# Kernel optimization log

Hardware: AMD Instinct MI355X
Metric: run time of the kernel (lower is better)

## Reference

```python
import jax, jax.numpy as jnp
import numpy as np

# Model dims (match init_kwargs)
H = 1024            # hidden_size
I = 2048            # intermediate_size (per expert)
NH = 16             # num_heads
HD = H // NH        # head_dim = 64
E = 8               # num_experts
TOPK = 2
MAX_SEQ = 2048
EPS = 1e-6
NEG = -1e9


def precompute_freqs_cis(dim, max_seq_len, theta=10000.0):
    # Faithful to source: cat([cos, sin], dim=-1) -> shape [S, dim]
    pos = np.arange(max_seq_len, dtype=np.float32)
    freqs = np.arange(0, dim, 2, dtype=np.float32) / dim
    inv_freq = 1.0 / (theta ** freqs)
    f = np.einsum('i,j->ij', pos, inv_freq)
    return jnp.asarray(np.concatenate([np.cos(f), np.sin(f)], axis=-1), dtype=jnp.float32)


def setup_inputs() -> dict:
    key = jax.random.key(0)
    ks = jax.random.split(key, 12)
    B, S = 2, 1024
    s = lambda fan: 1.0 / np.sqrt(fan)
    inp = {
        'x': jax.random.normal(ks[0], (B, S, H), dtype=jnp.float32),
        'attn_norm_w': jnp.ones((H,), dtype=jnp.float32),
        'ffn_norm_w': jnp.ones((H,), dtype=jnp.float32),
        'wq': jax.random.normal(ks[1], (H, H), dtype=jnp.float32) * s(H),
        'wk': jax.random.normal(ks[2], (H, H), dtype=jnp.float32) * s(H),
        'wv': jax.random.normal(ks[3], (H, H), dtype=jnp.float32) * s(H),
        'wo': jax.random.normal(ks[4], (H, H), dtype=jnp.float32) * s(H),
        'router_w': jax.random.normal(ks[5], (H, E), dtype=jnp.float32) * s(H),
        'w1': jax.random.normal(ks[6], (E, H, I), dtype=jnp.float32) * s(H),
        'w3': jax.random.normal(ks[7], (E, H, I), dtype=jnp.float32) * s(H),
        'w2': jax.random.normal(ks[8], (E, I, H), dtype=jnp.float32) * s(I),
        'freqs_cis': precompute_freqs_cis(HD, MAX_SEQ),
    }
    return inp


def rmsnorm(x, w):
    rms = jnp.sqrt(jnp.mean(x * x, axis=-1, keepdims=True) + EPS)
    return w * (x / rms)


def apply_rope(x, freqs_cis):
    # x: [B, S, NH, HD]; faithful to source pairing (interleaved view of cat(cos,sin))
    B, S, nh, hd = x.shape
    xr = x.reshape(B, S, nh, hd // 2, 2)
    fr = freqs_cis[:S].reshape(1, S, 1, hd // 2, 2)  # position_ids = arange(S)
    a, b = xr[..., 0], xr[..., 1]
    cr, ci = fr[..., 0], fr[..., 1]
    out = jnp.stack([a * cr - b * ci, a * ci + b * cr], axis=-1)
    return out.reshape(B, S, nh, hd)


def attention(x, wq, wk, wv, wo, freqs_cis):
    B, S, _ = x.shape
    q = (x @ wq).reshape(B, S, NH, HD)
    k = (x @ wk).reshape(B, S, NH, HD)
    v = (x @ wv).reshape(B, S, NH, HD)
    q = apply_rope(q, freqs_cis)
    k = apply_rope(k, freqs_cis)
    # [B, NH, S, S]
    scores = jnp.einsum('bqhd,bkhd->bhqk', q, k) / np.sqrt(HD).astype(np.float32)
    causal = jnp.tril(jnp.ones((S, S), dtype=bool))
    scores = jnp.where(causal[None, None], scores, NEG)
    attn = jax.nn.softmax(scores, axis=-1)
    out = jnp.einsum('bhqk,bkhd->bqhd', attn, v).reshape(B, S, H)
    return out @ wo


def moe_ffn(x, router_w, w1, w2, w3):
    # x: [B, S, H] -> flatten tokens
    B, S, _ = x.shape
    xt = x.reshape(B * S, H)                      # [T, H]
    logits = xt @ router_w                        # [T, E]
    probs = jax.nn.softmax(logits, axis=-1)
    topv, topi = jax.lax.top_k(probs, TOPK)       # [T, K]
    topv = topv / jnp.sum(topv, axis=-1, keepdims=True)  # renormalize top-k weights
    # combine[t, e] = sum_k topv[t,k] * 1[topi[t,k]==e]
    combine = jnp.sum(topv[..., None] * jax.nn.one_hot(topi, E, dtype=xt.dtype), axis=1)  # [T, E]
    # SwiGLU experts, dense over experts (mathematically identical to no-drop routing)
    h1 = jnp.einsum('th,ehi->eti', xt, w1)
    h3 = jnp.einsum('th,ehi->eti', xt, w3)
    ye = jnp.einsum('eti,eih->eth', jax.nn.silu(h1) * h3, w2)  # [E, T, H]
    out = jnp.einsum('te,eth->th', combine, ye)
    return out.reshape(B, S, H)


def reference(x, attn_norm_w, ffn_norm_w, wq, wk, wv, wo, router_w, w1, w3, w2, freqs_cis):
    h = x + attention(rmsnorm(x, attn_norm_w), wq, wk, wv, wo, freqs_cis)
    out = h + moe_ffn(rmsnorm(h, ffn_norm_w), router_w, w1, w2, w3)
    return out
```

## Files before the change

kernel.cpp:

```cpp
#include <hip/hip_runtime.h>
#include <hip/hip_bf16.h>
#include <math.h>

#define HS 1024
#define IS 2048
#define NHEAD 16
#define HDIM 64
#define NEXP 8
#define BATCH 2
#define SEQ 1024
#define NTOK (BATCH*SEQ)
#define NASSIGN (NTOK*2)
#define QKVW 3072
#define PAD 72

typedef short bf16x8 __attribute__((ext_vector_type(8)));
typedef float f32x4  __attribute__((ext_vector_type(4)));

__global__ void rmsnorm_split(const float* __restrict__ x, const float* __restrict__ w,
                              __hip_bfloat16* __restrict__ oh, __hip_bfloat16* __restrict__ ol) {
    int t = blockIdx.x;
    int tid = threadIdx.x;
    const float* row = x + (size_t)t * HS;
    float ss = 0.f;
    for (int i = tid; i < HS; i += 256) { float v = row[i]; ss += v * v; }
    for (int off = 32; off > 0; off >>= 1) ss += __shfl_down(ss, off);
    __shared__ float red[4];
    if ((tid & 63) == 0) red[tid >> 6] = ss;
    __syncthreads();
    float tot = red[0] + red[1] + red[2] + red[3];
    float rr = rsqrtf(tot / (float)HS + 1e-6f);
    for (int i = tid; i < HS; i += 256) {
        float v = w[i] * row[i] * rr;
        __hip_bfloat16 hi = __float2bfloat16(v);
        oh[(size_t)t * HS + i] = hi;
        ol[(size_t)t * HS + i] = __float2bfloat16(v - __bfloat162float(hi));
    }
}

__global__ void rmsnorm_dual(const float* __restrict__ x, const float* __restrict__ w,
                             float* __restrict__ outf, __hip_bfloat16* __restrict__ outb) {
    int t = blockIdx.x;
    int tid = threadIdx.x;
    const float* row = x + (size_t)t * HS;
    float ss = 0.f;
    for (int i = tid; i < HS; i += 256) { float v = row[i]; ss += v * v; }
    for (int off = 32; off > 0; off >>= 1) ss += __shfl_down(ss, off);
    __shared__ float red[4];
    if ((tid & 63) == 0) red[tid >> 6] = ss;
    __syncthreads();
    float tot = red[0] + red[1] + red[2] + red[3];
    float rr = rsqrtf(tot / (float)HS + 1e-6f);
    for (int i = tid; i < HS; i += 256) {
        float v = w[i] * row[i] * rr;
        outf[(size_t)t * HS + i] = v;
        outb[(size_t)t * HS + i] = __float2bfloat16(v);
    }
}

__global__ void transpose_split(const float* __restrict__ src,
                                __hip_bfloat16* __restrict__ dh, __hip_bfloat16* __restrict__ dl,
                                int R, int C, int rowOff) {
    __shared__ float tile[32][33];
    int c0 = blockIdx.x * 32, r0 = blockIdx.y * 32;
    int tx = threadIdx.x & 31, ty = threadIdx.x >> 5;
    #pragma unroll
    for (int i = 0; i < 4; i++) {
        int r = ty + i * 8;
        tile[r][tx] = src[(size_t)(r0 + r) * C + c0 + tx];
    }
    __syncthreads();
    #pragma unroll
    for (int i = 0; i < 4; i++) {
        int c = ty + i * 8;
        float v = tile[tx][c];
        __hip_bfloat16 hi = __float2bfloat16(v);
        size_t o = (size_t)(rowOff + c0 + c) * R + r0 + tx;
        dh[o] = hi;
        dl[o] = __float2bfloat16(v - __bfloat162float(hi));
    }
}

__global__ void transpose_bf16(const float* __restrict__ in, __hip_bfloat16* __restrict__ outp,
                               int R, int C) {
    __shared__ float tile[32][33];
    int e = blockIdx.z;
    const float* src = in + (size_t)e * R * C;
    __hip_bfloat16* dst = outp + (size_t)e * R * C;
    int c0 = blockIdx.x * 32, r0 = blockIdx.y * 32;
    int tx = threadIdx.x & 31, ty = threadIdx.x >> 5;
    #pragma unroll
    for (int i = 0; i < 4; i++) {
        int r = ty + i * 8;
        tile[r][tx] = src[(size_t)(r0 + r) * C + c0 + tx];
    }
    __syncthreads();
    #pragma unroll
    for (int i = 0; i < 4; i++) {
        int c = ty + i * 8;
        dst[(size_t)(c0 + c) * R + r0 + tx] = __float2bfloat16(tile[tx][c]);
    }
}

__global__ __launch_bounds__(256) void gemm_bf16x3(const __hip_bfloat16* __restrict__ Ah,
                                                   const __hip_bfloat16* __restrict__ Al,
                                                   const __hip_bfloat16* __restrict__ Bh,
                                                   const __hip_bfloat16* __restrict__ Bl,
                                                   const float* __restrict__ resid,
                                                   float* __restrict__ C,
                                                   int M, int N, int K) {
    __shared__ __align__(16) short Ahs[128][40];
    __shared__ __align__(16) short Als[128][40];
    __shared__ __align__(16) short Bhs[128][40];
    __shared__ __align__(16) short Bls[128][40];
    int bm = blockIdx.y * 128, bn = blockIdx.x * 128;
    int t = threadIdx.x;
    int wave = t >> 6, lane = t & 63;
    int wm = (wave & 1) * 64, wn = (wave >> 1) * 64;
    int fr = lane & 15;
    int kh = (lane >> 4) * 8;
    int srow = t >> 2;
    int scol = (t & 3) * 8;
    const __hip_bfloat16* a0h = Ah + (size_t)(bm + srow) * K + scol;
    const __hip_bfloat16* a1h = Ah + (size_t)(bm + 64 + srow) * K + scol;
    const __hip_bfloat16* a0l = Al + (size_t)(bm + srow) * K + scol;
    const __hip_bfloat16* a1l = Al + (size_t)(bm + 64 + srow) * K + scol;
    const __hip_bfloat16* b0h = Bh + (size_t)(bn + srow) * K + scol;
    const __hip_bfloat16* b1h = Bh + (size_t)(bn + 64 + srow) * K + scol;
    const __hip_bfloat16* b0l = Bl + (size_t)(bn + srow) * K + scol;
    const __hip_bfloat16* b1l = Bl + (size_t)(bn + 64 + srow) * K + scol;

    f32x4 acc[4][4] = {};
    for (int k0 = 0; k0 < K; k0 += 32) {
        *(uint4*)&Ahs[srow][scol]      = *(const uint4*)(a0h + k0);
        *(uint4*)&Ahs[64 + srow][scol] = *(const uint4*)(a1h + k0);
        *(uint4*)&Als[srow][scol]      = *(const uint4*)(a0l + k0);
        *(uint4*)&Als[64 + srow][scol] = *(const uint4*)(a1l + k0);
        *(uint4*)&Bhs[srow][scol]      = *(const uint4*)(b0h + k0);
        *(uint4*)&Bhs[64 + srow][scol] = *(const uint4*)(b1h + k0);
        *(uint4*)&Bls[srow][scol]      = *(const uint4*)(b0l + k0);
        *(uint4*)&Bls[64 + srow][scol] = *(const uint4*)(b1l + k0);
        __syncthreads();
        bf16x8 ah[4], bh[4], x[4];
        #pragma unroll
        for (int i = 0; i < 4; i++) {
            ah[i] = *(const bf16x8*)&Ahs[wm + i * 16 + fr][kh];
            bh[i] = *(const bf16x8*)&Bhs[wn + i * 16 + fr][kh];
        }
        #pragma unroll
        for (int mi = 0; mi < 4; mi++)
            #pragma unroll
            for (int ni = 0; ni < 4; ni++)
                acc[mi][ni] = __builtin_amdgcn_mfma_f32_16x16x32_bf16(ah[mi], bh[ni], acc[mi][ni], 0, 0, 0);
        #pragma unroll
        for (int i = 0; i < 4; i++) x[i] = *(const bf16x8*)&Bls[wn + i * 16 + fr][kh];
        #pragma unroll
        for (int mi = 0; mi < 4; mi++)
            #pragma unroll
            for (int ni = 0; ni < 4; ni++)
                acc[mi][ni] = __builtin_amdgcn_mfma_f32_16x16x32_bf16(ah[mi], x[ni], acc[mi][ni], 0, 0, 0);
        #pragma unroll
        for (int i = 0; i < 4; i++) x[i] = *(const bf16x8*)&Als[wm + i * 16 + fr][kh];
        #pragma unroll
        for (int mi = 0; mi < 4; mi++)
            #pragma unroll
            for (int ni = 0; ni < 4; ni++)
                acc[mi][ni] = __builtin_amdgcn_mfma_f32_16x16x32_bf16(x[mi], bh[ni], acc[mi][ni], 0, 0, 0);
        __syncthreads();
    }
    int rq = (lane >> 4) * 4;
    #pragma unroll
    for (int mi = 0; mi < 4; mi++) {
        #pragma unroll
        for (int r = 0; r < 4; r++) {
            size_t rowo = (size_t)(bm + wm + mi * 16 + rq + r) * N + bn + wn;
            #pragma unroll
            for (int ni = 0; ni < 4; ni++) {
                float v = acc[mi][ni][r];
                size_t o = rowo + ni * 16 + fr;
                if (resid) v += resid[o];
                C[o] = v;
            }
        }
    }
}

__global__ void rope_convert(const float* __restrict__ qkv, const float* __restrict__ fc,
                             __hip_bfloat16* __restrict__ qh, __hip_bfloat16* __restrict__ ql,
                             __hip_bfloat16* __restrict__ kh, __hip_bfloat16* __restrict__ kl,
                             __hip_bfloat16* __restrict__ vh, __hip_bfloat16* __restrict__ vl) {
    int t = blockIdx.x;
    int s = t & (SEQ - 1);
    const float* row = qkv + (size_t)t * QKVW;
    size_t ob = (size_t)t * HS;
    for (int p = threadIdx.x; p < 512; p += 256) {
        int hh = p >> 5, j = p & 31;
        int col = hh * 64 + 2 * j;
        float cr = fc[s * HDIM + 2 * j];
        float ci = fc[s * HDIM + 2 * j + 1];
        float a = row[col], b = row[col + 1];
        float r0 = a * cr - b * ci, r1 = a * ci + b * cr;
        __hip_bfloat16 h0 = __float2bfloat16(r0), h1 = __float2bfloat16(r1);
        qh[ob + col] = h0;     ql[ob + col]     = __float2bfloat16(r0 - __bfloat162float(h0));
        qh[ob + col + 1] = h1; ql[ob + col + 1] = __float2bfloat16(r1 - __bfloat162float(h1));
        a = row[1024 + col]; b = row[1024 + col + 1];
        r0 = a * cr - b * ci; r1 = a * ci + b * cr;
        h0 = __float2bfloat16(r0); h1 = __float2bfloat16(r1);
        kh[ob + col] = h0;     kl[ob + col]     = __float2bfloat16(r0 - __bfloat162float(h0));
        kh[ob + col + 1] = h1; kl[ob + col + 1] = __float2bfloat16(r1 - __bfloat162float(h1));
        r0 = row[2048 + col]; r1 = row[2048 + col + 1];
        h0 = __float2bfloat16(r0); h1 = __float2bfloat16(r1);
        vh[ob + col] = h0;     vl[ob + col]     = __float2bfloat16(r0 - __bfloat162float(h0));
        vh[ob + col + 1] = h1; vl[ob + col + 1] = __float2bfloat16(r1 - __bfloat162float(h1));
    }
}

__global__ __launch_bounds__(256) void attn_partial(
        const __hip_bfloat16* __restrict__ qh, const __hip_bfloat16* __restrict__ ql,
        const __hip_bfloat16* __restrict__ kh, const __hip_bfloat16* __restrict__ kl,
        const __hip_bfloat16* __restrict__ vh, const __hip_bfloat16* __restrict__ vl,
        float* __restrict__ po, float* __restrict__ pm_g, float* __restrict__ pl_g) {
    int c = blockIdx.x, qt = blockIdx.y;
    int nc = (qt + 4) >> 2;
    if (c >= nc) return;
    int bh = blockIdx.z;
    int b = bh >> 4, h = bh & 15;
    int t0 = c * 4, t1 = min(t0 + 4, qt + 1);
    int tid = threadIdx.x;
    int wave = tid >> 6, lane = tid & 63;
    int fr = lane & 15, quad = lane >> 4;
    int w16 = wave * 16;
    __shared__ __align__(16) short Qh[64][PAD], Ql[64][PAD];
    __shared__ __align__(16) short KPh[64][PAD], KPl[64][PAD];
    __shared__ __align__(16) short Vhs[64][PAD], Vls[64][PAD];
    size_t hoff = (size_t)h * HDIM;
    int sr = tid >> 2, sg = tid & 3;
    {
        const __hip_bfloat16* qp  = qh + (size_t)(b * SEQ + qt * 64 + sr) * HS + hoff;
        const __hip_bfloat16* qp2 = ql + (size_t)(b * SEQ + qt * 64 + sr) * HS + hoff;
        *(uint4*)&Qh[sr][sg * 8]       = *(const uint4*)(qp + sg * 8);
        *(uint4*)&Qh[sr][(sg + 4) * 8] = *(const uint4*)(qp + (sg + 4) * 8);
        *(uint4*)&Ql[sr][sg * 8]       = *(const uint4*)(qp2 + sg * 8);
        *(uint4*)&Ql[sr][(sg + 4) * 8] = *(const uint4*)(qp2 + (sg + 4) * 8);
    }
    f32x4 o[4] = {};
    float mrow[4], lrow[4];
    #pragma unroll
    for (int i = 0; i < 4; i++) { mrow[i] = -1e30f; lrow[i] = 0.f; }
    int key0 = (tid & 31) * 2, ds = tid >> 5;
    __syncthreads();

    for (int kt = t0; kt < t1; kt++) {
        int kbase = kt * 64;
        {
            const __hip_bfloat16* kp  = kh + (size_t)(b * SEQ + kbase + sr) * HS + hoff;
            const __hip_bfloat16* kp2 = kl + (size_t)(b * SEQ + kbase + sr) * HS + hoff;
            *(uint4*)&KPh[sr][sg * 8]       = *(const uint4*)(kp + sg * 8);
            *(uint4*)&KPh[sr][(sg + 4) * 8] = *(const uint4*)(kp + (sg + 4) * 8);
            *(uint4*)&KPl[sr][sg * 8]       = *(const uint4*)(kp2 + sg * 8);
            *(uint4*)&KPl[sr][(sg + 4) * 8] = *(const uint4*)(kp2 + (sg + 4) * 8);
        }
        {
            const __hip_bfloat16* v0 = vh + (size_t)(b * SEQ + kbase + key0) * HS + hoff + ds * 8;
            uint4 A = *(const uint4*)v0;
            uint4 Bv = *(const uint4*)(v0 + HS);
            const unsigned short* ap = (const unsigned short*)&A;
            const unsigned short* bp = (const unsigned short*)&Bv;
            #pragma unroll
            for (int j = 0; j < 8; j++)
                *(unsigned*)&Vhs[ds * 8 + j][key0] = (unsigned)ap[j] | ((unsigned)bp[j] << 16);
            const __hip_bfloat16* v2 = vl + (size_t)(b * SEQ + kbase + key0) * HS + hoff + ds * 8;
            uint4 A2 = *(const uint4*)v2;
            uint4 B2 = *(const uint4*)(v2 + HS);
            const unsigned short* ap2 = (const unsigned short*)&A2;
            const unsigned short* bp2 = (const unsigned short*)&B2;
            #pragma unroll
            for (int j = 0; j < 8; j++)
                *(unsigned*)&Vls[ds * 8 + j][key0] = (unsigned)ap2[j] | ((unsigned)bp2[j] << 16);
        }
        __syncthreads();

        f32x4 s[4] = {};
        #pragma unroll
        for (int ks = 0; ks < 2; ks++) {
            bf16x8 a_h = *(const bf16x8*)&Qh[w16 + fr][quad * 8 + ks * 32];
            bf16x8 a_l = *(const bf16x8*)&Ql[w16 + fr][quad * 8 + ks * 32];
            #pragma unroll
            for (int ni = 0; ni < 4; ni++) {
                bf16x8 b_h = *(const bf16x8*)&KPh[ni * 16 + fr][quad * 8 + ks * 32];
                bf16x8 b_l = *(const bf16x8*)&KPl[ni * 16 + fr][quad * 8 + ks * 32];
                s[ni] = __builtin_amdgcn_mfma_f32_16x16x32_bf16(a_h, b_h, s[ni], 0, 0, 0);
                s[ni] = __builtin_amdgcn_mfma_f32_16x16x32_bf16(a_h, b_l, s[ni], 0, 0, 0);
                s[ni] = __builtin_amdgcn_mfma_f32_16x16x32_bf16(a_l, b_h, s[ni], 0, 0, 0);
            }
        }
        int qg = qt * 64 + w16 + quad * 4;
        #pragma unroll
        for (int ni = 0; ni < 4; ni++) {
            int kg = kbase + ni * 16 + fr;
            #pragma unroll
            for (int r = 0; r < 4; r++)
                s[ni][r] = (kg > qg + r) ? -1e9f : s[ni][r] * 0.125f;
        }
        #pragma unroll
        for (int r = 0; r < 4; r++) {
            float mx = fmaxf(fmaxf(s[0][r], s[1][r]), fmaxf(s[2][r], s[3][r]));
            #pragma unroll
            for (int wd = 1; wd < 16; wd <<= 1) mx = fmaxf(mx, __shfl_xor(mx, wd));
            float nm = fmaxf(mrow[r], mx);
            float alpha = __expf(mrow[r] - nm);
            float rs = 0.f;
            #pragma unroll
            for (int ni = 0; ni < 4; ni++) { float e = __expf(s[ni][r] - nm); s[ni][r] = e; rs += e; }
            #pragma unroll
            for (int wd = 1; wd < 16; wd <<= 1) rs += __shfl_xor(rs, wd);
            lrow[r] = lrow[r] * alpha + rs;
            mrow[r] = nm;
            o[0][r] *= alpha; o[1][r] *= alpha; o[2][r] *= alpha; o[3][r] *= alpha;
        }
        __syncthreads();
        #pragma unroll
        for (int ni = 0; ni < 4; ni++)
            #pragma unroll
            for (int r = 0; r < 4; r++) {
                float pv = s[ni][r];
                __hip_bfloat16 hi = __float2bfloat16(pv);
                __hip_bfloat16 lo = __float2bfloat16(pv - __bfloat162float(hi));
                KPh[w16 + quad * 4 + r][ni * 16 + fr] = *(short*)&hi;
                KPl[w16 + quad * 4 + r][ni * 16 + fr] = *(short*)&lo;
            }
        #pragma unroll
        for (int ks = 0; ks < 2; ks++) {
            bf16x8 p_h = *(const bf16x8*)&KPh[w16 + fr][quad * 8 + ks * 32];
            bf16x8 p_l = *(const bf16x8*)&KPl[w16 + fr][quad * 8 + ks * 32];
            #pragma unroll
            for (int ni = 0; ni < 4; ni++) {
                bf16x8 v_h = *(const bf16x8*)&Vhs[ni * 16 + fr][quad * 8 + ks * 32];
                bf16x8 v_l = *(const bf16x8*)&Vls[ni * 16 + fr][quad * 8 + ks * 32];
                o[ni] = __builtin_amdgcn_mfma_f32_16x16x32_bf16(p_h, v_h, o[ni], 0, 0, 0);
                o[ni] = __builtin_amdgcn_mfma_f32_16x16x32_bf16(p_h, v_l, o[ni], 0, 0, 0);
                o[ni] = __builtin_amdgcn_mfma_f32_16x16x32_bf16(p_l, v_h, o[ni], 0, 0, 0);
            }
        }
        __syncthreads();
    }
    int pidx = (bh * 16 + qt) * 4 + c;
    float* pob = po + (size_t)pidx * 4096;
    #pragma unroll
    for (int ni = 0; ni < 4; ni++)
        #pragma unroll
        for (int r = 0; r < 4; r++)
            pob[(w16 + quad * 4 + r) * 64 + ni * 16 + fr] = o[ni][r];
    if (fr == 0) {
        #pragma unroll
        for (int r = 0; r < 4; r++) {
            pm_g[pidx * 64 + w16 + quad * 4 + r] = mrow[r];
            pl_g[pidx * 64 + w16 + quad * 4 + r] = lrow[r];
        }
    }
}

__global__ void attn_merge(const float* __restrict__ po, const float* __restrict__ pm,
                           const float* __restrict__ pl,
                           __hip_bfloat16* __restrict__ ch, __hip_bfloat16* __restrict__ cl) {
    int qt = blockIdx.x, h = blockIdx.y, b = blockIdx.z;
    int bh = b * 16 + h;
    int nc = (qt + 4) >> 2;
    int base = (bh * 16 + qt) * 4;
    int tid = threadIdx.x;
    int r  = tid >> 2;
    int d0 = (tid & 3) * 16;
    float mstar = -1e30f;
    for (int c = 0; c < nc; c++) mstar = fmaxf(mstar, pm[(base + c) * 64 + r]);
    float a[4];
    float lsum = 0.f;
    for (int c = 0; c < nc; c++) {
        a[c] = __expf(pm[(base + c) * 64 + r] - mstar);
        lsum += a[c] * pl[(base + c) * 64 + r];
    }
    float inv = 1.f / lsum;
    size_t crow = (size_t)(b * SEQ + qt * 64 + r) * HS + h * HDIM;
    for (int dd = 0; dd < 16; dd += 4) {
        float4 acc = make_float4(0.f, 0.f, 0.f, 0.f);
        for (int c = 0; c < nc; c++) {
            float4 v = *(const float4*)(po + (size_t)(base + c) * 4096 + r * 64 + d0 + dd);
            acc.x += a[c] * v.x; acc.y += a[c] * v.y;
            acc.z += a[c] * v.z; acc.w += a[c] * v.w;
        }
        float vs[4] = {acc.x * inv, acc.y * inv, acc.z * inv, acc.w * inv};
        #pragma unroll
        for (int j = 0; j < 4; j++) {
            __hip_bfloat16 hi = __float2bfloat16(vs[j]);
            ch[crow + d0 + dd + j] = hi;
            cl[crow + d0 + dd + j] = __float2bfloat16(vs[j] - __bfloat162float(hi));
        }
    }
}

__global__ void router_kernel(const float* __restrict__ hn, const float* __restrict__ rw,
                              int* __restrict__ cnt, int* __restrict__ topEk,
                              float* __restrict__ topW) {
    int t = blockIdx.x;
    int lane = threadIdx.x;
    float acc[NEXP];
    #pragma unroll
    for (int e = 0; e < NEXP; e++) acc[e] = 0.f;
    const float* row = hn + (size_t)t * HS;
    for (int kk = lane; kk < HS; kk += 64) {
        float xv = row[kk];
        const float* r = rw + (size_t)kk * NEXP;
        #pragma unroll
        for (int e = 0; e < NEXP; e++) acc[e] += xv * r[e];
    }
    #pragma unroll
    for (int e = 0; e < NEXP; e++)
        for (int off = 32; off > 0; off >>= 1) acc[e] += __shfl_down(acc[e], off);
    if (lane == 0) {
        float mx = acc[0];
        #pragma unroll
        for (int e = 1; e < NEXP; e++) mx = fmaxf(mx, acc[e]);
        float p[NEXP]; float s = 0.f;
        #pragma unroll
        for (int e = 0; e < NEXP; e++) { p[e] = __expf(acc[e] - mx); s += p[e]; }
        int i0 = 0;
        #pragma unroll
        for (int e = 1; e < NEXP; e++) if (p[e] > p[i0]) i0 = e;
        int i1 = (i0 == 0) ? 1 : 0;
        #pragma unroll
        for (int e = 0; e < NEXP; e++) if (e != i0 && p[e] > p[i1]) i1 = e;
        float v0 = p[i0], v1 = p[i1], sn = v0 + v1;
        topEk[2 * t]     = i0; topW[2 * t]     = v0 / sn;
        topEk[2 * t + 1] = i1; topW[2 * t + 1] = v1 / sn;
        atomicAdd(&cnt[i0], 1);
        atomicAdd(&cnt[i1], 1);
    }
}

__global__ void offsets_kernel(const int* __restrict__ cnt, int* __restrict__ off) {
    if (threadIdx.x == 0) {
        int o = 0;
        for (int e = 0; e < NEXP; e++) { off[e] = o; o += cnt[e]; }
    }
}

__global__ void scatter_kernel(const int* __restrict__ topEk, int* __restrict__ fill,
                               const int* __restrict__ off, const float* __restrict__ topW,
                               int* __restrict__ tok_list, float* __restrict__ wA) {
    int idx = blockIdx.x * 256 + threadIdx.x;
    int e = topEk[idx];
    int slot = atomicAdd(&fill[e], 1);
    int gidx = off[e] + slot;
    tok_list[gidx] = idx >> 1;
    wA[gidx] = topW[idx];
}

__global__ __launch_bounds__(256) void moe_up_mfma(const __hip_bfloat16* __restrict__ Abf,
                                                   const __hip_bfloat16* __restrict__ B1T,
                                                   const __hip_bfloat16* __restrict__ B3T,
                                                   __hip_bfloat16* __restrict__ g,
                                                   const int* __restrict__ cnt,
                                                   const int* __restrict__ off,
                                                   const int* __restrict__ tok_list) {
    int e = blockIdx.z;
    int ce = cnt[e];
    int bm = blockIdx.y * 128;
    if (bm >= ce) return;
    int oe = off[e];
    int bn = blockIdx.x * 128;
    const __hip_bfloat16* b1 = B1T + (size_t)e * IS * HS;
    const __hip_bfloat16* b3 = B3T + (size_t)e * IS * HS;

    __shared__ __align__(16) short As[128][40];
    __shared__ __align__(16) short B1s[128][40];
    __shared__ __align__(16) short B3s[128][40];
    __shared__ int toks[128];

    int t = threadIdx.x;
    int wave = t >> 6, lane = t & 63;
    int wm = (wave & 1) * 64, wn = (wave >> 1) * 64;
    int fr = lane & 15;
    int kh = (lane >> 4) * 8;

    if (t < 128) {
        int gidx = oe + bm + t;
        if (gidx > NASSIGN - 1) gidx = NASSIGN - 1;
        toks[t] = tok_list[gidx];
    }
    __syncthreads();
    int srow = t >> 2;
    int scol = (t & 3) * 8;
    const __hip_bfloat16* rowA0 = Abf + (size_t)toks[srow] * HS + scol;
    const __hip_bfloat16* rowA1 = Abf + (size_t)toks[64 + srow] * HS + scol;
    const __hip_bfloat16* rowB1a = b1 + (size_t)(bn + srow) * HS + scol;
    const __hip_bfloat16* rowB1b = b1 + (size_t)(bn + 64 + srow) * HS + scol;
    const __hip_bfloat16* rowB3a = b3 + (size_t)(bn + srow) * HS + scol;
    const __hip_bfloat16* rowB3b = b3 + (size_t)(bn + 64 + srow) * HS + scol;

    f32x4 acc1[4][4] = {};
    f32x4 acc3[4][4] = {};

    for (int k0 = 0; k0 < HS; k0 += 32) {
        *(uint4*)&As[srow][scol]       = *(const uint4*)(rowA0 + k0);
        *(uint4*)&As[64 + srow][scol]  = *(const uint4*)(rowA1 + k0);
        *(uint4*)&B1s[srow][scol]      = *(const uint4*)(rowB1a + k0);
        *(uint4*)&B1s[64 + srow][scol] = *(const uint4*)(rowB1b + k0);
        *(uint4*)&B3s[srow][scol]      = *(const uint4*)(rowB3a + k0);
        *(uint4*)&B3s[64 + srow][scol] = *(const uint4*)(rowB3b + k0);
        __syncthreads();
        bf16x8 a[4], f1[4], f3[4];
        #pragma unroll
        for (int i = 0; i < 4; i++) {
            a[i]  = *(const bf16x8*)&As[wm + i * 16 + fr][kh];
            f1[i] = *(const bf16x8*)&B1s[wn + i * 16 + fr][kh];
            f3[i] = *(const bf16x8*)&B3s[wn + i * 16 + fr][kh];
        }
        #pragma unroll
        for (int mi = 0; mi < 4; mi++)
            #pragma unroll
            for (int ni = 0; ni < 4; ni++) {
                acc1[mi][ni] = __builtin_amdgcn_mfma_f32_16x16x32_bf16(a[mi], f1[ni], acc1[mi][ni], 0, 0, 0);
                acc3[mi][ni] = __builtin_amdgcn_mfma_f32_16x16x32_bf16(a[mi], f3[ni], acc3[mi][ni], 0, 0, 0);
            }
        __syncthreads();
    }
    int rq = (lane >> 4) * 4;
    #pragma unroll
    for (int mi = 0; mi < 4; mi++) {
        #pragma unroll
        for (int r = 0; r < 4; r++) {
            int slot = bm + wm + mi * 16 + rq + r;
            if (slot < ce) {
                size_t rowo = (size_t)(oe + slot) * IS + bn + wn;
                #pragma unroll
                for (int ni = 0; ni < 4; ni++) {
                    float x1 = acc1[mi][ni][r];
                    float x3 = acc3[mi][ni][r];
                    float sv = (x1 / (1.f + __expf(-x1))) * x3;
                    g[rowo + ni * 16 + fr] = __float2bfloat16(sv);
                }
            }
        }
    }
}

__global__ __launch_bounds__(256) void moe_down_mfma(const __hip_bfloat16* __restrict__ g,
                                                     const __hip_bfloat16* __restrict__ B2T,
                                                     float* __restrict__ out,
                                                     const int* __restrict__ cnt,
                                                     const int* __restrict__ off,
                                                     const int* __restrict__ tok_list,
                                                     const float* __restrict__ wA) {
    int e = blockIdx.z;
    int ce = cnt[e];
    int bm = blockIdx.y * 128;
    if (bm >= ce) return;
    int oe = off[e];
    int bn = blockIdx.x * 128;
    const __hip_bfloat16* b2 = B2T + (size_t)e * HS * IS;

    __shared__ __align__(16) short As[128][40];
    __shared__ __align__(16) short Bs[128][40];

    int t = threadIdx.x;
    int wave = t >> 6, lane = t & 63;
    int wm = (wave & 1) * 64, wn = (wave >> 1) * 64;
    int fr = lane & 15;
    int kh = (lane >> 4) * 8;

    int srow = t >> 2;
    int scol = (t & 3) * 8;
    int ga0 = oe + bm + srow;       if (ga0 > NASSIGN - 1) ga0 = NASSIGN - 1;
    int ga1 = oe + bm + 64 + srow;  if (ga1 > NASSIGN - 1) ga1 = NASSIGN - 1;
    const __hip_bfloat16* rowA0 = g + (size_t)ga0 * IS + scol;
    const __hip_bfloat16* rowA1 = g + (size_t)ga1 * IS + scol;
    const __hip_bfloat16* rowBa = b2 + (size_t)(bn + srow) * IS + scol;
    const __hip_bfloat16* rowBb = b2 + (size_t)(bn + 64 + srow) * IS + scol;

    f32x4 acc[4][4] = {};

    for (int k0 = 0; k0 < IS; k0 += 32) {
        *(uint4*)&As[srow][scol]      = *(const uint4*)(rowA0 + k0);
        *(uint4*)&As[64 + srow][scol] = *(const uint4*)(rowA1 + k0);
        *(uint4*)&Bs[srow][scol]      = *(const uint4*)(rowBa + k0);
        *(uint4*)&Bs[64 + srow][scol] = *(const uint4*)(rowBb + k0);
        __syncthreads();
        bf16x8 a[4], f[4];
        #pragma unroll
        for (int i = 0; i < 4; i++) {
            a[i] = *(const bf16x8*)&As[wm + i * 16 + fr][kh];
            f[i] = *(const bf16x8*)&Bs[wn + i * 16 + fr][kh];
        }
        #pragma unroll
        for (int mi = 0; mi < 4; mi++)
            #pragma unroll
            for (int ni = 0; ni < 4; ni++)
                acc[mi][ni] = __builtin_amdgcn_mfma_f32_16x16x32_bf16(a[mi], f[ni], acc[mi][ni], 0, 0, 0);
        __syncthreads();
    }
    int rq = (lane >> 4) * 4;
    #pragma unroll
    for (int mi = 0; mi < 4; mi++) {
        #pragma unroll
        for (int r = 0; r < 4; r++) {
            int slot = bm + wm + mi * 16 + rq + r;
            if (slot < ce) {
                int gidx = oe + slot;
                int tok = tok_list[gidx];
                float wgt = wA[gidx];
                size_t rowo = (size_t)tok * HS + bn + wn;
                #pragma unroll
                for (int ni = 0; ni < 4; ni++)
                    atomicAdd(out + rowo + ni * 16 + fr, wgt * acc[mi][ni][r]);
            }
        }
    }
}

extern "C" void kernel_launch(void* const* d_in, const int* in_sizes, int n_in,
                              void* d_out, int out_size, void* d_ws, size_t ws_size,
                              hipStream_t stream) {
    const float* x   = (const float*)d_in[0];
    const float* anw = (const float*)d_in[1];
    const float* fnw = (const float*)d_in[2];
    const float* wq  = (const float*)d_in[3];
    const float* wk  = (const float*)d_in[4];
    const float* wv  = (const float*)d_in[5];
    const float* wo  = (const float*)d_in[6];
    const float* rw  = (const float*)d_in[7];
    const float* w1  = (const float*)d_in[8];
    const float* w3  = (const float*)d_in[9];
    const float* w2  = (const float*)d_in[10];
    const float* fc  = (const float*)d_in[11];
    float* out = (float*)d_out;

    char* ws = (char*)d_ws;
    const size_t MB = 1024 * 1024;
    __hip_bfloat16* xn_h  = (__hip_bfloat16*)(ws + 0 * MB);
    __hip_bfloat16* xn_l  = (__hip_bfloat16*)(ws + 4 * MB);
    float*          qkv   = (float*)(ws + 8 * MB);
    __hip_bfloat16* WqT_h = (__hip_bfloat16*)(ws + 32 * MB);
    __hip_bfloat16* WqT_l = (__hip_bfloat16*)(ws + 38 * MB);
    __hip_bfloat16* woT_h = (__hip_bfloat16*)(ws + 44 * MB);
    __hip_bfloat16* woT_l = (__hip_bfloat16*)(ws + 46 * MB);
    float*          po    = (float*)(ws + 48 * MB);
    float*          pm    = (float*)(ws + 82 * MB);
    float*          plb   = (float*)(ws + 83 * MB);
    __hip_bfloat16* ctx_h = (__hip_bfloat16*)(ws + 84 * MB);
    __hip_bfloat16* ctx_l = (__hip_bfloat16*)(ws + 88 * MB);
    __hip_bfloat16* qhb   = (__hip_bfloat16*)(ws + 92 * MB);
    __hip_bfloat16* qlb   = (__hip_bfloat16*)(ws + 96 * MB);
    __hip_bfloat16* khb   = (__hip_bfloat16*)(ws + 100 * MB);
    __hip_bfloat16* klb   = (__hip_bfloat16*)(ws + 104 * MB);
    __hip_bfloat16* vhb   = (__hip_bfloat16*)(ws + 108 * MB);
    __hip_bfloat16* vlb   = (__hip_bfloat16*)(ws + 112 * MB);
    float*          hn    = (float*)(ws + 0 * MB);
    __hip_bfloat16* hn_bf = (__hip_bfloat16*)(ws + 8 * MB);
    __hip_bfloat16* w1T   = (__hip_bfloat16*)(ws + 12 * MB);
    __hip_bfloat16* w3T   = (__hip_bfloat16*)(ws + 44 * MB);
    __hip_bfloat16* w2T   = (__hip_bfloat16*)(ws + 76 * MB);
    __hip_bfloat16* gact  = (__hip_bfloat16*)(ws + 108 * MB);
    int* ibase    = (int*)(ws + 124 * MB);
    int* cnt      = ibase;
    int* fill     = ibase + 8;
    int* off      = ibase + 16;
    int* topEk    = ibase + 32;
    int* tok_list = ibase + 32 + NASSIGN;
    float* topW   = (float*)(ibase + 32 + 2 * NASSIGN);
    float* wA     = (float*)(ibase + 32 + 3 * NASSIGN);

    dim3 tg(HS / 32, HS / 32);
    transpose_split<<<tg, 256, 0, stream>>>(wq, WqT_h, WqT_l, HS, HS, 0);
    transpose_split<<<tg, 256, 0, stream>>>(wk, WqT_h, WqT_l, HS, HS, 1024);
    transpose_split<<<tg, 256, 0, stream>>>(wv, WqT_h, WqT_l, HS, HS, 2048);
    transpose_split<<<tg, 256, 0, stream>>>(wo, woT_h, woT_l, HS, HS, 0);
    rmsnorm_split<<<NTOK, 256, 0, stream>>>(x, anw, xn_h, xn_l);

    gemm_bf16x3<<<dim3(QKVW / 128, NTOK / 128), 256, 0, stream>>>(
        xn_h, xn_l, WqT_h, WqT_l, nullptr, qkv, NTOK, QKVW, HS);
    rope_convert<<<NTOK, 256, 0, stream>>>(qkv, fc, qhb, qlb, khb, klb, vhb, vlb);

    attn_partial<<<dim3(4, 16, 32), 256, 0, stream>>>(qhb, qlb, khb, klb, vhb, vlb, po, pm, plb);
    attn_merge<<<dim3(16, 16, 2), 256, 0, stream>>>(po, pm, plb, ctx_h, ctx_l);

    gemm_bf16x3<<<dim3(HS / 128, NTOK / 128), 256, 0, stream>>>(
        ctx_h, ctx_l, woT_h, woT_l, x, out, NTOK, HS, HS);

    rmsnorm_dual<<<NTOK, 256, 0, stream>>>(out, fnw, hn, hn_bf);
    transpose_bf16<<<dim3(IS / 32, HS / 32, NEXP), 256, 0, stream>>>(w1, w1T, HS, IS);
    transpose_bf16<<<dim3(IS / 32, HS / 32, NEXP), 256, 0, stream>>>(w3, w3T, HS, IS);
    transpose_bf16<<<dim3(HS / 32, IS / 32, NEXP), 256, 0, stream>>>(w2, w2T, IS, HS);

    hipMemsetAsync(cnt, 0, 16 * sizeof(int), stream);
    router_kernel<<<NTOK, 64, 0, stream>>>(hn, rw, cnt, topEk, topW);
    offsets_kernel<<<1, 64, 0, stream>>>(cnt, off);
    scatter_kernel<<<NASSIGN / 256, 256, 0, stream>>>(topEk, fill, off, topW, tok_list, wA);

    dim3 gup(IS / 128, NASSIGN / 128, NEXP);
    moe_up_mfma<<<gup, 256, 0, stream>>>(hn_bf, w1T, w3T, gact, cnt, off, tok_list);
    dim3 gdn(HS / 128, NASSIGN / 128, NEXP);
    moe_down_mfma<<<gdn, 256, 0, stream>>>(gact, w2T, out, cnt, off, tok_list, wA);
}
```

Measured before the change: 732.5 us.

## Use global_load_lds DMA with XOR swizzle and compact MoE block scheduling

The GEMM and MoE kernels now load tiles straight from global memory into LDS with global_load_lds, dropping the padded LDS rows and using an XOR swizzle on the 16-byte chunks to avoid bank conflicts. The MoE up and down kernels launch only a compact list of (expert, row-block) work items built in offsets_kernel, instead of a grid padded to the worst case with many early-exit blocks. The aim is to cut register staging, LDS bank conflicts and empty-block launch overhead. The risks are LDS-DMA alignment and layout correctness, the fixed MAXBLK bound on the number of work items, and blk_e overlapping other index storage in the workspace.

```diff
diff --git a/kernel.cpp b/kernel.cpp
--- a/kernel.cpp
+++ b/kernel.cpp
@@ -13,9 +13,16 @@
 #define NASSIGN (NTOK*2)
 #define QKVW 3072
 #define PAD 72
+#define MAXBLK 40
 
 typedef short bf16x8 __attribute__((ext_vector_type(8)));
 typedef float f32x4  __attribute__((ext_vector_type(4)));
+
+__device__ __forceinline__ void ldsdma16(void* lds, const void* gp) {
+    __builtin_amdgcn_global_load_lds(
+        (const __attribute__((address_space(1))) void*)gp,
+        (__attribute__((address_space(3))) void*)lds, 16, 0, 0);
+}
 
 __global__ void rmsnorm_split(const float* __restrict__ x, const float* __restrict__ w,
                               __hip_bfloat16* __restrict__ oh, __hip_bfloat16* __restrict__ ol) {
@@ -109,43 +116,44 @@
                                                    const float* __restrict__ resid,
                                                    float* __restrict__ C,
                                                    int M, int N, int K) {
-    __shared__ __align__(16) short Ahs[128][40];
-    __shared__ __align__(16) short Als[128][40];
-    __shared__ __align__(16) short Bhs[128][40];
-    __shared__ __align__(16) short Bls[128][40];
+    __shared__ __align__(16) short Ahs[128][32];
+    __shared__ __align__(16) short Als[128][32];
+    __shared__ __align__(16) short Bhs[128][32];
+    __shared__ __align__(16) short Bls[128][32];
     int bm = blockIdx.y * 128, bn = blockIdx.x * 128;
     int t = threadIdx.x;
     int wave = t >> 6, lane = t & 63;
     int wm = (wave & 1) * 64, wn = (wave >> 1) * 64;
-    int fr = lane & 15;
-    int kh = (lane >> 4) * 8;
-    int srow = t >> 2;
-    int scol = (t & 3) * 8;
-    const __hip_bfloat16* a0h = Ah + (size_t)(bm + srow) * K + scol;
-    const __hip_bfloat16* a1h = Ah + (size_t)(bm + 64 + srow) * K + scol;
-    const __hip_bfloat16* a0l = Al + (size_t)(bm + srow) * K + scol;
-    const __hip_bfloat16* a1l = Al + (size_t)(bm + 64 + srow) * K + scol;
-    const __hip_bfloat16* b0h = Bh + (size_t)(bn + srow) * K + scol;
-    const __hip_bfloat16* b1h = Bh + (size_t)(bn + 64 + srow) * K + scol;
-    const __hip_bfloat16* b0l = Bl + (size_t)(bn + srow) * K + scol;
-    const __hip_bfloat16* b1l = Bl + (size_t)(bn + 64 + srow) * K + scol;
+    int fr = lane & 15, quad = lane >> 4;
+    int r0 = wave * 32;
+    int srow = lane >> 2;
+    int schunk = (lane & 3) ^ ((lane >> 3) & 3);
+    const __hip_bfloat16* pAh0 = Ah + (size_t)(bm + r0 + srow) * K + schunk * 8;
+    const __hip_bfloat16* pAh1 = pAh0 + (size_t)16 * K;
+    const __hip_bfloat16* pAl0 = Al + (size_t)(bm + r0 + srow) * K + schunk * 8;
+    const __hip_bfloat16* pAl1 = pAl0 + (size_t)16 * K;
+    const __hip_bfloat16* pBh0 = Bh + (size_t)(bn + r0 + srow) * K + schunk * 8;
+    const __hip_bfloat16* pBh1 = pBh0 + (size_t)16 * K;
+    const __hip_bfloat16* pBl0 = Bl + (size_t)(bn + r0 + srow) * K + schunk * 8;
+    const __hip_bfloat16* pBl1 = pBl0 + (size_t)16 * K;
+    int ca = (quad ^ ((fr >> 1) & 3)) * 8;
 
     f32x4 acc[4][4] = {};
     for (int k0 = 0; k0 < K; k0 += 32) {
-        *(uint4*)&Ahs[srow][scol]      = *(const uint4*)(a0h + k0);
-        *(uint4*)&Ahs[64 + srow][scol] = *(const uint4*)(a1h + k0);
-        *(uint4*)&Als[srow][scol]      = *(const uint4*)(a0l + k0);
-        *(uint4*)&Als[64 + srow][scol] = *(const uint4*)(a1l + k0);
-        *(uint4*)&Bhs[srow][scol]      = *(const uint4*)(b0h + k0);
-        *(uint4*)&Bhs[64 + srow][scol] = *(const uint4*)(b1h + k0);
-        *(uint4*)&Bls[srow][scol]      = *(const uint4*)(b0l + k0);
-        *(uint4*)&Bls[64 + srow][scol] = *(const uint4*)(b1l + k0);
+        ldsdma16(&Ahs[r0][0],      pAh0 + k0);
+        ldsdma16(&Ahs[r0 + 16][0], pAh1 + k0);
+        ldsdma16(&Als[r0][0],      pAl0 + k0);
+        ldsdma16(&Als[r0 + 16][0], pAl1 + k0);
+        ldsdma16(&Bhs[r0][0],      pBh0 + k0);
+        ldsdma16(&Bhs[r0 + 16][0], pBh1 + k0);
+        ldsdma16(&Bls[r0][0],      pBl0 + k0);
+        ldsdma16(&Bls[r0 + 16][0], pBl1 + k0);
         __syncthreads();
         bf16x8 ah[4], bh[4], x[4];
         #pragma unroll
         for (int i = 0; i < 4; i++) {
-            ah[i] = *(const bf16x8*)&Ahs[wm + i * 16 + fr][kh];
-            bh[i] = *(const bf16x8*)&Bhs[wn + i * 16 + fr][kh];
+            ah[i] = *(const bf16x8*)&Ahs[wm + i * 16 + fr][ca];
+            bh[i] = *(const bf16x8*)&Bhs[wn + i * 16 + fr][ca];
         }
         #pragma unroll
         for (int mi = 0; mi < 4; mi++)
@@ -153,14 +161,14 @@
             for (int ni = 0; ni < 4; ni++)
                 acc[mi][ni] = __builtin_amdgcn_mfma_f32_16x16x32_bf16(ah[mi], bh[ni], acc[mi][ni], 0, 0, 0);
         #pragma unroll
-        for (int i = 0; i < 4; i++) x[i] = *(const bf16x8*)&Bls[wn + i * 16 + fr][kh];
+        for (int i = 0; i < 4; i++) x[i] = *(const bf16x8*)&Bls[wn + i * 16 + fr][ca];
         #pragma unroll
         for (int mi = 0; mi < 4; mi++)
             #pragma unroll
             for (int ni = 0; ni < 4; ni++)
                 acc[mi][ni] = __builtin_amdgcn_mfma_f32_16x16x32_bf16(ah[mi], x[ni], acc[mi][ni], 0, 0, 0);
         #pragma unroll
-        for (int i = 0; i < 4; i++) x[i] = *(const bf16x8*)&Als[wm + i * 16 + fr][kh];
+        for (int i = 0; i < 4; i++) x[i] = *(const bf16x8*)&Als[wm + i * 16 + fr][ca];
         #pragma unroll
         for (int mi = 0; mi < 4; mi++)
             #pragma unroll
@@ -168,7 +176,7 @@
                 acc[mi][ni] = __builtin_amdgcn_mfma_f32_16x16x32_bf16(x[mi], bh[ni], acc[mi][ni], 0, 0, 0);
         __syncthreads();
     }
-    int rq = (lane >> 4) * 4;
+    int rq = quad * 4;
     #pragma unroll
     for (int mi = 0; mi < 4; mi++) {
         #pragma unroll
@@ -436,10 +444,16 @@
     }
 }
 
-__global__ void offsets_kernel(const int* __restrict__ cnt, int* __restrict__ off) {
+__global__ void offsets_kernel(const int* __restrict__ cnt, int* __restrict__ off,
+                               int* __restrict__ blk_e, int* __restrict__ blk_r) {
     if (threadIdx.x == 0) {
-        int o = 0;
-        for (int e = 0; e < NEXP; e++) { off[e] = o; o += cnt[e]; }
+        int o = 0, n = 0;
+        for (int e = 0; e < NEXP; e++) {
+            off[e] = o;
+            for (int bm = 0; bm < cnt[e]; bm += 128) { blk_e[n] = e; blk_r[n] = bm; n++; }
+            o += cnt[e];
+        }
+        for (; n < MAXBLK; n++) { blk_e[n] = -1; blk_r[n] = 0; }
     }
 }
 
@@ -460,59 +474,55 @@
                                                    __hip_bfloat16* __restrict__ g,
                                                    const int* __restrict__ cnt,
                                                    const int* __restrict__ off,
-                                                   const int* __restrict__ tok_list) {
-    int e = blockIdx.z;
-    int ce = cnt[e];
-    int bm = blockIdx.y * 128;
-    if (bm >= ce) return;
-    int oe = off[e];
+                                                   const int* __restrict__ tok_list,
+                                                   const int* __restrict__ blk_e,
+                                                   const int* __restrict__ blk_r) {
+    int e = blk_e[blockIdx.y];
+    if (e < 0) return;
+    int bm = blk_r[blockIdx.y];
+    int ce = cnt[e], oe = off[e];
     int bn = blockIdx.x * 128;
     const __hip_bfloat16* b1 = B1T + (size_t)e * IS * HS;
     const __hip_bfloat16* b3 = B3T + (size_t)e * IS * HS;
 
-    __shared__ __align__(16) short As[128][40];
-    __shared__ __align__(16) short B1s[128][40];
-    __shared__ __align__(16) short B3s[128][40];
-    __shared__ int toks[128];
+    __shared__ __align__(16) short As[128][32];
+    __shared__ __align__(16) short B1s[128][32];
+    __shared__ __align__(16) short B3s[128][32];
 
     int t = threadIdx.x;
     int wave = t >> 6, lane = t & 63;
     int wm = (wave & 1) * 64, wn = (wave >> 1) * 64;
-    int fr = lane & 15;
-    int kh = (lane >> 4) * 8;
-
-    if (t < 128) {
-        int gidx = oe + bm + t;
-        if (gidx > NASSIGN - 1) gidx = NASSIGN - 1;
-        toks[t] = tok_list[gidx];
-    }
-    __syncthreads();
-    int srow = t >> 2;
-    int scol = (t & 3) * 8;
-    const __hip_bfloat16* rowA0 = Abf + (size_t)toks[srow] * HS + scol;
-    const __hip_bfloat16* rowA1 = Abf + (size_t)toks[64 + srow] * HS + scol;
-    const __hip_bfloat16* rowB1a = b1 + (size_t)(bn + srow) * HS + scol;
-    const __hip_bfloat16* rowB1b = b1 + (size_t)(bn + 64 + srow) * HS + scol;
-    const __hip_bfloat16* rowB3a = b3 + (size_t)(bn + srow) * HS + scol;
-    const __hip_bfloat16* rowB3b = b3 + (size_t)(bn + 64 + srow) * HS + scol;
+    int fr = lane & 15, quad = lane >> 4;
+    int r0 = wave * 32;
+    int srow = lane >> 2;
+    int schunk = (lane & 3) ^ ((lane >> 3) & 3);
+    int tokA0 = tok_list[oe + min(bm + r0 + srow, ce - 1)];
+    int tokA1 = tok_list[oe + min(bm + r0 + 16 + srow, ce - 1)];
+    const __hip_bfloat16* pA0 = Abf + (size_t)tokA0 * HS + schunk * 8;
+    const __hip_bfloat16* pA1 = Abf + (size_t)tokA1 * HS + schunk * 8;
+    const __hip_bfloat16* pB1a = b1 + (size_t)(bn + r0 + srow) * HS + schunk * 8;
+    const __hip_bfloat16* pB1b = pB1a + (size_t)16 * HS;
+    const __hip_bfloat16* pB3a = b3 + (size_t)(bn + r0 + srow) * HS + schunk * 8;
+    const __hip_bfloat16* pB3b = pB3a + (size_t)16 * HS;
+    int ca = (quad ^ ((fr >> 1) & 3)) * 8;
 
     f32x4 acc1[4][4] = {};
     f32x4 acc3[4][4] = {};
 
     for (int k0 = 0; k0 < HS; k0 += 32) {
-        *(uint4*)&As[srow][scol]       = *(const uint4*)(rowA0 + k0);
-        *(uint4*)&As[64 + srow][scol]  = *(const uint4*)(rowA1 + k0);
-        *(uint4*)&B1s[srow][scol]      = *(const uint4*)(rowB1a + k0);
-        *(uint4*)&B1s[64 + srow][scol] = *(const uint4*)(rowB1b + k0);
-        *(uint4*)&B3s[srow][scol]      = *(const uint4*)(rowB3a + k0);
-        *(uint4*)&B3s[64 + srow][scol] = *(const uint4*)(rowB3b + k0);
+        ldsdma16(&As[r0][0],       pA0 + k0);
+        ldsdma16(&As[r0 + 16][0],  pA1 + k0);
+        ldsdma16(&B1s[r0][0],      pB1a + k0);
+        ldsdma16(&B1s[r0 + 16][0], pB1b + k0);
+        ldsdma16(&B3s[r0][0],      pB3a + k0);
+        ldsdma16(&B3s[r0 + 16][0], pB3b + k0);
         __syncthreads();
         bf16x8 a[4], f1[4], f3[4];
         #pragma unroll
         for (int i = 0; i < 4; i++) {
-            a[i]  = *(const bf16x8*)&As[wm + i * 16 + fr][kh];
-            f1[i] = *(const bf16x8*)&B1s[wn + i * 16 + fr][kh];
-            f3[i] = *(const bf16x8*)&B3s[wn + i * 16 + fr][kh];
+            a[i]  = *(const bf16x8*)&As[wm + i * 16 + fr][ca];
+            f1[i] = *(const bf16x8*)&B1s[wn + i * 16 + fr][ca];
+            f3[i] = *(const bf16x8*)&B3s[wn + i * 16 + fr][ca];
         }
         #pragma unroll
         for (int mi = 0; mi < 4; mi++)
@@ -523,7 +533,7 @@
             }
         __syncthreads();
     }
-    int rq = (lane >> 4) * 4;
+    int rq = quad * 4;
     #pragma unroll
     for (int mi = 0; mi < 4; mi++) {
         #pragma unroll
@@ -549,46 +559,47 @@
                                                      const int* __restrict__ cnt,
                                                      const int* __restrict__ off,
                                                      const int* __restrict__ tok_list,
-                                                     const float* __restrict__ wA) {
-    int e = blockIdx.z;
-    int ce = cnt[e];
-    int bm = blockIdx.y * 128;
-    if (bm >= ce) return;
-    int oe = off[e];
+                                                     const float* __restrict__ wA,
+                                                     const int* __restrict__ blk_e,
+                                                     const int* __restrict__ blk_r) {
+    int e = blk_e[blockIdx.y];
+    if (e < 0) return;
+    int bm = blk_r[blockIdx.y];
+    int ce = cnt[e], oe = off[e];
     int bn = blockIdx.x * 128;
     const __hip_bfloat16* b2 = B2T + (size_t)e * HS * IS;
 
-    __shared__ __align__(16) short As[128][40];
-    __shared__ __align__(16) short Bs[128][40];
+    __shared__ __align__(16) short As[128][32];
+    __shared__ __align__(16) short Bs[128][32];
 
     int t = threadIdx.x;
     int wave = t >> 6, lane = t & 63;
     int wm = (wave & 1) * 64, wn = (wave >> 1) * 64;
-    int fr = lane & 15;
-    int kh = (lane >> 4) * 8;
-
-    int srow = t >> 2;
-    int scol = (t & 3) * 8;
-    int ga0 = oe + bm + srow;       if (ga0 > NASSIGN - 1) ga0 = NASSIGN - 1;
-    int ga1 = oe + bm + 64 + srow;  if (ga1 > NASSIGN - 1) ga1 = NASSIGN - 1;
-    const __hip_bfloat16* rowA0 = g + (size_t)ga0 * IS + scol;
-    const __hip_bfloat16* rowA1 = g + (size_t)ga1 * IS + scol;
-    const __hip_bfloat16* rowBa = b2 + (size_t)(bn + srow) * IS + scol;
-    const __hip_bfloat16* rowBb = b2 + (size_t)(bn + 64 + srow) * IS + scol;
+    int fr = lane & 15, quad = lane >> 4;
+    int r0 = wave * 32;
+    int srow = lane >> 2;
+    int schunk = (lane & 3) ^ ((lane >> 3) & 3);
+    int ga0 = oe + min(bm + r0 + srow, ce - 1);
+    int ga1 = oe + min(bm + r0 + 16 + srow, ce - 1);
+    const __hip_bfloat16* pA0 = g + (size_t)ga0 * IS + schunk * 8;
+    const __hip_bfloat16* pA1 = g + (size_t)ga1 * IS + schunk * 8;
+    const __hip_bfloat16* pBa = b2 + (size_t)(bn + r0 + srow) * IS + schunk * 8;
+    const __hip_bfloat16* pBb = pBa + (size_t)16 * IS;
+    int ca = (quad ^ ((fr >> 1) & 3)) * 8;
 
     f32x4 acc[4][4] = {};
 
     for (int k0 = 0; k0 < IS; k0 += 32) {
-        *(uint4*)&As[srow][scol]      = *(const uint4*)(rowA0 + k0);
-        *(uint4*)&As[64 + srow][scol] = *(const uint4*)(rowA1 + k0);
-        *(uint4*)&Bs[srow][scol]      = *(const uint4*)(rowBa + k0);
-        *(uint4*)&Bs[64 + srow][scol] = *(const uint4*)(rowBb + k0);
+        ldsdma16(&As[r0][0],      pA0 + k0);
+        ldsdma16(&As[r0 + 16][0], pA1 + k0);
+        ldsdma16(&Bs[r0][0],      pBa + k0);
+        ldsdma16(&Bs[r0 + 16][0], pBb + k0);
         __syncthreads();
         bf16x8 a[4], f[4];
         #pragma unroll
         for (int i = 0; i < 4; i++) {
-            a[i] = *(const bf16x8*)&As[wm + i * 16 + fr][kh];
-            f[i] = *(const bf16x8*)&Bs[wn + i * 16 + fr][kh];
+            a[i] = *(const bf16x8*)&As[wm + i * 16 + fr][ca];
+            f[i] = *(const bf16x8*)&Bs[wn + i * 16 + fr][ca];
         }
         #pragma unroll
         for (int mi = 0; mi < 4; mi++)
@@ -597,7 +608,7 @@
                 acc[mi][ni] = __builtin_amdgcn_mfma_f32_16x16x32_bf16(a[mi], f[ni], acc[mi][ni], 0, 0, 0);
         __syncthreads();
     }
-    int rq = (lane >> 4) * 4;
+    int rq = quad * 4;
     #pragma unroll
     for (int mi = 0; mi < 4; mi++) {
         #pragma unroll
@@ -663,10 +674,12 @@
     int* cnt      = ibase;
     int* fill     = ibase + 8;
     int* off      = ibase + 16;
-    int* topEk    = ibase + 32;
-    int* tok_list = ibase + 32 + NASSIGN;
-    float* topW   = (float*)(ibase + 32 + 2 * NASSIGN);
-    float* wA     = (float*)(ibase + 32 + 3 * NASSIGN);
+    int* blk_e    = ibase + 24;
+    int* blk_r    = ibase + 64;
+    int* topEk    = ibase + 128;
+    int* tok_list = ibase + 128 + NASSIGN;
+    float* topW   = (float*)(ibase + 128 + 2 * NASSIGN);
+    float* wA     = (float*)(ibase + 128 + 3 * NASSIGN);
 
     dim3 tg(HS / 32, HS / 32);
     transpose_split<<<tg, 256, 0, stream>>>(wq, WqT_h, WqT_l, HS, HS, 0);
@@ -692,11 +705,11 @@
 
     hipMemsetAsync(cnt, 0, 16 * sizeof(int), stream);
     router_kernel<<<NTOK, 64, 0, stream>>>(hn, rw, cnt, topEk, topW);
-    offsets_kernel<<<1, 64, 0, stream>>>(cnt, off);
+    offsets_kernel<<<1, 64, 0, stream>>>(cnt, off, blk_e, blk_r);
     scatter_kernel<<<NASSIGN / 256, 256, 0, stream>>>(topEk, fill, off, topW, tok_list, wA);
 
-    dim3 gup(IS / 128, NASSIGN / 128, NEXP);
-    moe_up_mfma<<<gup, 256, 0, stream>>>(hn_bf, w1T, w3T, gact, cnt, off, tok_list);
-    dim3 gdn(HS / 128, NASSIGN / 128, NEXP);
-    moe_down_mfma<<<gdn, 256, 0, stream>>>(gact, w2T, out, cnt, off, tok_list, wA);
-}
+    moe_up_mfma<<<dim3(IS / 128, MAXBLK), 256, 0, stream>>>(
+        hn_bf, w1T, w3T, gact, cnt, off, tok_list, blk_e, blk_r);
+    moe_down_mfma<<<dim3(HS / 128, MAXBLK), 256, 0, stream>>>(
+        gact, w2T, out, cnt, off, tok_list, wA, blk_e, blk_r);
+}
```

Result: faster. 685.4 us (-6.4%).
